# Performance work log

Hardware: AMD Instinct MI355X
Metric: run time of the kernel (lower is better)

## Reference

```python
import jax, jax.numpy as jnp
import numpy as np

N_EMBD = 1024
N_HEADS = 16
HEAD_DIM = N_EMBD // N_HEADS


def setup_inputs() -> dict:
    key = jax.random.key(0)
    k0, k1, k2, k3, k4 = jax.random.split(key, 5)
    scale = 1.0 / np.sqrt(N_EMBD)
    x = jax.random.normal(k0, (2, 2048, N_EMBD), dtype=jnp.float32)
    # nn.Linear(n_embd, 3*n_embd): weight [3d, d], bias [3d]
    w_qkv = jax.random.normal(k1, (3 * N_EMBD, N_EMBD), dtype=jnp.float32) * scale
    b_qkv = jax.random.normal(k2, (3 * N_EMBD,), dtype=jnp.float32) * scale
    w_proj = jax.random.normal(k3, (N_EMBD, N_EMBD), dtype=jnp.float32) * scale
    b_proj = jax.random.normal(k4, (N_EMBD,), dtype=jnp.float32) * scale
    return {"x": x, "w_qkv": w_qkv, "b_qkv": b_qkv, "w_proj": w_proj, "b_proj": b_proj}


def reference(x, w_qkv, b_qkv, w_proj, b_proj):
    b, l, d = x.shape
    h, f = N_HEADS, HEAD_DIM
    qkv = x @ w_qkv.T + b_qkv                      # [b, l, 3d]
    # rearrange 'b l (c h f) -> c b h l f'
    qkv = qkv.reshape(b, l, 3, h, f)
    q = jnp.transpose(qkv[:, :, 0], (0, 2, 1, 3))  # [b, h, l, f]
    k = jnp.transpose(qkv[:, :, 1], (0, 2, 1, 3))
    v = jnp.transpose(qkv[:, :, 2], (0, 2, 1, 3))
    scores = jnp.einsum('bhqf,bhkf->bhqk', q, k) / jnp.sqrt(jnp.float32(f))
    att = jax.nn.softmax(scores, axis=-1)          # [b, h, l, l]
    y = jnp.einsum('bhqk,bhkf->bhqf', att, v)      # [b, h, l, f]
    y = jnp.transpose(y, (0, 2, 1, 3)).reshape(b, l, d)  # 'b h l f -> b l (h f)'
    return y @ w_proj.T + b_proj
```

## Files before the change

### kernel.cpp

```cpp
#include <hip/hip_runtime.h>
#include <hip/hip_bf16.h>
#include <stdint.h>


typedef unsigned short u16;
typedef __attribute__((ext_vector_type(8))) short short8;
typedef __attribute__((ext_vector_type(4))) float f32x4;
typedef __attribute__((ext_vector_type(16))) float f32x16;
typedef __attribute__((ext_vector_type(4))) unsigned int u32x4;

#define MFMA16(a, b, c) __builtin_amdgcn_mfma_f32_16x16x32_bf16((a), (b), (c), 0, 0, 0)
#define MFMA32(a, b, c) __builtin_amdgcn_mfma_f32_32x32x16_bf16((a), (b), (c), 0, 0, 0)

__device__ __forceinline__ u16 f2bf(float x) {
  union { float f; uint32_t u; } v; v.f = x;
  uint32_t r = v.u + 0x7FFFu + ((v.u >> 16) & 1u);
  return (u16)(r >> 16);
}

__device__ __forceinline__ float fexp2(float x) {
#if __has_builtin(__builtin_amdgcn_exp2f)
  return __builtin_amdgcn_exp2f(x);
#else
  return exp2f(x);
#endif
}

__device__ __forceinline__ uint32_t pkbf(float lo, float hi) {
  uint32_t a = __builtin_bit_cast(uint32_t, lo) + 0x8000u;
  uint32_t b = __builtin_bit_cast(uint32_t, hi) + 0x8000u;
  return __builtin_amdgcn_perm(b, a, 0x07060302u);
}

__device__ __forceinline__ void gload16(const void* g, void* l) {
  __builtin_amdgcn_global_load_lds((const __attribute__((address_space(1))) void*)g,
                                   (__attribute__((address_space(3))) void*)l, 16, 0, 0);
}

__global__ __launch_bounds__(256) void cvt_all(const float* __restrict__ x,
                                               const float* __restrict__ wq,
                                               const float* __restrict__ wp,
                                               u16* __restrict__ xb,
                                               u16* __restrict__ wqb,
                                               u16* __restrict__ wpb) {
  int i = blockIdx.x * 256 + threadIdx.x;
  const float* s; u16* d; int off;
  if (i < 1048576) { s = x; d = xb; off = i; }
  else if (i < 1835008) { s = wq; d = wqb; off = i - 1048576; }
  else { s = wp; d = wpb; off = i - 1835008; }
  float4 f = reinterpret_cast<const float4*>(s)[off];
  ushort4 o;
  o.x = f2bf(f.x); o.y = f2bf(f.y); o.z = f2bf(f.z); o.w = f2bf(f.w);
  reinterpret_cast<ushort4*>(d)[off] = o;
}

template <int EPI>
__global__ __launch_bounds__(256, 4) void gemm_bt(const u16* __restrict__ A,
                                                  const u16* __restrict__ B,
                                                  const float* __restrict__ bias,
                                                  u16* __restrict__ outb,
                                                  float* __restrict__ outf,
                                                  int M, int N, int K) {
  __shared__ u16 smem[16384];
  const int tid = threadIdx.x;
  const int lane = tid & 63;
  const int wid = tid >> 6;
  const int bn = blockIdx.x, bm = blockIdx.y;
  const int row0 = bm * 128, col0 = bn * 128;
  const int wr = wid >> 1, wc = wid & 1;
  const int fr = lane & 15, fq = lane >> 4;

  f32x4 acc[4][4];
  #pragma unroll
  for (int m = 0; m < 4; m++)
    #pragma unroll
    for (int n = 0; n < 4; n++)
      #pragma unroll
      for (int j = 0; j < 4; j++) acc[m][n][j] = 0.f;

  const int cB = tid + 256;
  const int rA1 = tid >> 2, rA2 = cB >> 2;
  const int lA1 = (tid & 3) ^ ((tid >> 3) & 3);
  const int lA2 = (cB & 3) ^ ((cB >> 3) & 3);
  const size_t ga1 = (size_t)rA1 * K + lA1 * 8;
  const size_t ga2 = (size_t)rA2 * K + lA2 * 8;
  const int d1 = tid * 8, d2 = cB * 8;
  const u16* Ab = A + (size_t)row0 * K;
  const u16* Bb = B + (size_t)col0 * K;

  const int sl = (fq ^ ((fr >> 1) & 3)) * 8;
  const int niter = K >> 5;

  {
    u16* s = smem;
    gload16(Ab + ga1, s + d1);
    gload16(Ab + ga2, s + d2);
    gload16(Bb + ga1, s + 4096 + d1);
    gload16(Bb + ga2, s + 4096 + d2);
  }
  __syncthreads();

  for (int t = 0; t < niter; t++) {
    if (t + 1 < niter) {
      u16* s = smem + ((t + 1) & 1) * 8192;
      const size_t k0 = (size_t)(t + 1) * 32;
      gload16(Ab + ga1 + k0, s + d1);
      gload16(Ab + ga2 + k0, s + d2);
      gload16(Bb + ga1 + k0, s + 4096 + d1);
      gload16(Bb + ga2 + k0, s + 4096 + d2);
    }
    const u16* sa = smem + (t & 1) * 8192;
    const u16* sb = sa + 4096;
    short8 a[4], b[4];
    #pragma unroll
    for (int m = 0; m < 4; m++)
      a[m] = *(const short8*)&sa[(wr * 64 + m * 16 + fr) * 32 + sl];
    #pragma unroll
    for (int n = 0; n < 4; n++)
      b[n] = *(const short8*)&sb[(wc * 64 + n * 16 + fr) * 32 + sl];
    __builtin_amdgcn_s_setprio(1);
    #pragma unroll
    for (int m = 0; m < 4; m++)
      #pragma unroll
      for (int n = 0; n < 4; n++)
        acc[m][n] = MFMA16(a[m], b[n], acc[m][n]);
    __builtin_amdgcn_s_setprio(0);
    __syncthreads();
  }

  if (EPI == 0) {
    if (bn < 16) {
      #pragma unroll
      for (int m = 0; m < 4; m++) {
        #pragma unroll
        for (int n = 0; n < 4; n++) {
          #pragma unroll
          for (int j = 0; j < 4; j++) {
            int r = row0 + wr * 64 + m * 16 + fq * 4 + j;
            int c = col0 + wc * 64 + n * 16 + fr;
            float v = acc[m][n][j] + bias[c];
            int d = c & 1023, h = d >> 6, f = d & 63;
            int bb = r >> 11, ll = r & 2047;
            int bhh = bb * 16 + h;
            if (bn < 8) {
              outb[((size_t)bhh * 2048 + ll) * 64 + f] = f2bf(v * 0.18033688f);
            } else {
              outb[4194304u + ((size_t)bhh * 2048 + ll) * 64 + f] = f2bf(v);
            }
          }
        }
      }
    } else {
      u16* sC = smem;
      #pragma unroll
      for (int m = 0; m < 4; m++) {
        #pragma unroll
        for (int n = 0; n < 4; n++) {
          int c_local = wc * 64 + n * 16 + fr;
          int r_base = wr * 64 + m * 16 + fq * 4;
          float bi = bias[col0 + c_local];
          uint2 w;
          w.x = pkbf(acc[m][n][0] + bi, acc[m][n][1] + bi);
          w.y = pkbf(acc[m][n][2] + bi, acc[m][n][3] + bi);
          *(uint2*)&sC[c_local * 128 + (r_base ^ ((c_local & 7) << 3))] = w;
        }
      }
      __syncthreads();
      const int h0 = (col0 - 2048) >> 6;
      const int ll0 = row0 & 2047;
      const int bb = row0 >> 11;
      #pragma unroll
      for (int it = 0; it < 8; it++) {
        int chunk = tid + it * 256;
        int row_c = chunk >> 4, off = chunk & 15;
        short8 v = *(const short8*)&sC[row_c * 128 + ((off * 8) ^ ((row_c & 7) << 3))];
        int h = h0 + (row_c >> 6), f = row_c & 63;
        *(short8*)&outb[8388608u + ((size_t)((bb * 16 + h) * 64 + f)) * 2048 + ll0 + off * 8] = v;
      }
    }
  } else {
    #pragma unroll
    for (int m = 0; m < 4; m++)
      #pragma unroll
      for (int n = 0; n < 4; n++)
        #pragma unroll
        for (int j = 0; j < 4; j++) {
          int r = row0 + wr * 64 + m * 16 + fq * 4 + j;
          int c = col0 + wc * 64 + n * 16 + fr;
          outf[(size_t)r * N + c] = acc[m][n][j] + bias[c];
        }
  }
}

__device__ __forceinline__ void softpack1(const f32x16& st, float& lp,
                                          short8& paA, short8& paB) {
  float e[16];
  #pragma unroll
  for (int r = 0; r < 16; r++) e[r] = fexp2(st[r]);
  #pragma unroll
  for (int r = 0; r < 16; r++) lp += e[r];
  #pragma unroll
  for (int cc = 0; cc < 2; cc++) {
    uint32_t g0 = pkbf(e[8 * cc + 0], e[8 * cc + 1]);
    uint32_t g1 = pkbf(e[8 * cc + 2], e[8 * cc + 3]);
    uint32_t g2 = pkbf(e[8 * cc + 4], e[8 * cc + 5]);
    uint32_t g3 = pkbf(e[8 * cc + 6], e[8 * cc + 7]);
    asm volatile("v_permlane32_swap_b32 %0, %1" : "+v"(g0), "+v"(g2));
    asm volatile("v_permlane32_swap_b32 %0, %1" : "+v"(g1), "+v"(g3));
    u32x4 t;
    t[0] = g0; t[1] = g1; t[2] = g2; t[3] = g3;
    if (cc == 0) paA = __builtin_bit_cast(short8, t);
    else paB = __builtin_bit_cast(short8, t);
  }
}

__global__ __launch_bounds__(256, 4) void attn_kernel(const u16* __restrict__ qg,
                                                      const u16* __restrict__ kg,
                                                      const u16* __restrict__ vtg,
                                                      u16* __restrict__ y) {
  __shared__ u16 sStage[16384];
  __shared__ float sL2[64];
  const int x = blockIdx.x;
  const int bh = (x & 7) * 4 + (x >> 8);
  const int qt = (x >> 3) & 31;
  const int tid = threadIdx.x, l = tid & 63, wid = tid >> 6;
  const int qs = wid & 1, kh = wid >> 1;
  const int col = l & 31, hi = l >> 5;
  const size_t base = (size_t)bh * 131072;
  const u16* qp = qg + base;
  const u16* kp = kg + base + (size_t)kh * 1024 * 64;
  const u16* vp = vtg + base + (size_t)kh * 1024;
  const int qrow = qt * 64 + qs * 32;

  short8 qf[4];
  #pragma unroll
  for (int kk = 0; kk < 4; kk++)
    qf[kk] = *(const short8*)&qp[(size_t)(qrow + col) * 64 + kk * 16 + hi * 8];

  const int kc_row = tid >> 3;
  const int kc_src = kc_row * 64 + (((tid & 7) ^ ((tid >> 3) & 7)) * 8);
  const int vc_row = tid >> 2;
  const int vc_src = vc_row * 2048 + (((tid & 3) ^ ((tid >> 3) & 3)) * 8);
  const int kdst = tid * 8;
  const int vdst = 2048 + tid * 8;
  u16* S0 = sStage;
  u16* S1 = sStage + 8192;
  const u16* kp0 = kg + base;
  const u16* kp1 = kg + base + 65536;
  const u16* vp0 = vtg + base;
  const u16* vp1 = vtg + base + 1024;

  f32x16 o0, o1;
  float lp = 0.f;
  #pragma unroll
  for (int r = 0; r < 16; r++) { o0[r] = 0.f; o1[r] = 0.f; }

  const int krsw = (col & 7) << 3;
  const int vrsw = ((col >> 1) & 3) << 3;

  gload16(kp0 + kc_src, S0 + kdst);
  gload16(vp0 + vc_src, S0 + vdst);
  gload16(kp1 + kc_src, S1 + kdst);
  gload16(vp1 + vc_src, S1 + vdst);

  const u16* Sw = sStage + kh * 8192;
  int sel = 0;
  for (int t = 0; t < 32; t++) {
    __syncthreads();
    if (t + 1 < 32) {
      const size_t ko = (size_t)(t + 1) * 32 * 64;
      const int vo = (t + 1) * 32;
      u16* b0 = S0 + (sel ^ 1) * 4096;
      u16* b1 = S1 + (sel ^ 1) * 4096;
      gload16(kp0 + ko + kc_src, b0 + kdst);
      gload16(vp0 + vo + vc_src, b0 + vdst);
      gload16(kp1 + ko + kc_src, b1 + kdst);
      gload16(vp1 + vo + vc_src, b1 + vdst);
    }
    const u16* S = Sw + sel * 4096;

    f32x16 st;
    #pragma unroll
    for (int r = 0; r < 16; r++) st[r] = 0.f;
    __builtin_amdgcn_s_setprio(1);
    #pragma unroll
    for (int kk = 0; kk < 4; kk++) {
      short8 kb = *(const short8*)&S[col * 64 + ((kk * 16 + hi * 8) ^ krsw)];
      st = MFMA32(kb, qf[kk], st);
    }
    __builtin_amdgcn_s_setprio(0);

    short8 pa[2];
    softpack1(st, lp, pa[0], pa[1]);

    __builtin_amdgcn_s_setprio(1);
    #pragma unroll
    for (int c = 0; c < 2; c++) {
      short8 vb0 = *(const short8*)&S[2048 + col * 32 + ((c * 16 + hi * 8) ^ vrsw)];
      short8 vb1 = *(const short8*)&S[2048 + (32 + col) * 32 + ((c * 16 + hi * 8) ^ vrsw)];
      o0 = MFMA32(pa[c], vb0, o0);
      o1 = MFMA32(pa[c], vb1, o1);
    }
    __builtin_amdgcn_s_setprio(0);
    sel ^= 1;
  }

  __syncthreads();
  float* sM = (float*)sStage;
  float* sMl = sM + 4096;
  if (kh == 1) {
    #pragma unroll
    for (int r = 0; r < 16; r++) {
      sM[qs * 2048 + r * 64 + l] = o0[r];
      sM[qs * 2048 + (16 + r) * 64 + l] = o1[r];
    }
    sMl[qs * 64 + l] = lp;
  }
  __syncthreads();
  if (kh == 0) {
    #pragma unroll
    for (int r = 0; r < 16; r++) {
      o0[r] += sM[qs * 2048 + r * 64 + l];
      o1[r] += sM[qs * 2048 + (16 + r) * 64 + l];
    }
    lp += sMl[qs * 64 + l];
    float lsum = lp + __shfl_xor(lp, 32);
    if (l < 32) sL2[qs * 32 + col] = 1.0f / lsum;
    __builtin_amdgcn_s_waitcnt(0);
    const int b = bh >> 4, hh = bh & 15;
    #pragma unroll
    for (int fvt = 0; fvt < 2; fvt++) {
      #pragma unroll
      for (int r = 0; r < 16; r++) {
        int q = (r & 3) + 8 * (r >> 2) + 4 * hi;
        float li = sL2[qs * 32 + q];
        float v = (fvt == 0 ? o0[r] : o1[r]) * li;
        y[((size_t)(b * 2048 + qrow + q)) * 1024 + hh * 64 + fvt * 32 + col] = f2bf(v);
      }
    }
  }
}

extern "C" void kernel_launch(void* const* d_in, const int* in_sizes, int n_in,
                              void* d_out, int out_size, void* d_ws, size_t ws_size,
                              hipStream_t stream) {
  const float* x = (const float*)d_in[0];
  const float* w_qkv = (const float*)d_in[1];
  const float* b_qkv = (const float*)d_in[2];
  const float* w_proj = (const float*)d_in[3];
  const float* b_proj = (const float*)d_in[4];
  float* out = (float*)d_out;

  u16* ws = (u16*)d_ws;
  u16* xb = ws;
  u16* wq = xb + 4194304;
  u16* wp = wq + 3145728;
  u16* qb = wp + 1048576;
  u16* kb = qb + 4194304;
  u16* vb = kb + 4194304;
  u16* yb = vb + 4194304;

  cvt_all<<<8192, 256, 0, stream>>>(x, w_qkv, w_proj, xb, wq, wp);

  gemm_bt<0><<<dim3(24, 32), 256, 0, stream>>>(xb, wq, b_qkv, qb, nullptr, 4096, 3072, 1024);

  attn_kernel<<<1024, 256, 0, stream>>>(qb, kb, vb, yb);

  gemm_bt<1><<<dim3(8, 32), 256, 0, stream>>>(yb, wp, b_proj, nullptr, out, 4096, 1024, 1024);
}
```

Before: 121.8 us.

## Use four-slot K/V ring buffer and software-pipeline QK with softmax

Replaces the double-buffered K/V staging with a four-slot ring in shared memory. The loop now processes two tiles per iteration with one barrier, issuing the score MFMA for the next tile before the current softmax/PV so matrix work overlaps exp and packing. The row-sum accumulation is also rewritten as a balanced tree to shorten the dependency chain. Shared memory per block doubles, which can lower how many blocks fit per CU under the launch bound of four.

New measurement: 125.4 us. 3.0% more time.

```diff
diff --git a/kernel.cpp b/kernel.cpp
--- a/kernel.cpp
+++ b/kernel.cpp
@@ -197,8 +197,11 @@
   float e[16];
   #pragma unroll
   for (int r = 0; r < 16; r++) e[r] = fexp2(st[r]);
-  #pragma unroll
-  for (int r = 0; r < 16; r++) lp += e[r];
+  float s0 = (e[0] + e[1]) + (e[2] + e[3]);
+  float s1 = (e[4] + e[5]) + (e[6] + e[7]);
+  float s2 = (e[8] + e[9]) + (e[10] + e[11]);
+  float s3 = (e[12] + e[13]) + (e[14] + e[15]);
+  lp += (s0 + s1) + (s2 + s3);
   #pragma unroll
   for (int cc = 0; cc < 2; cc++) {
     uint32_t g0 = pkbf(e[8 * cc + 0], e[8 * cc + 1]);
@@ -218,7 +221,7 @@
                                                       const u16* __restrict__ kg,
                                                       const u16* __restrict__ vtg,
                                                       u16* __restrict__ y) {
-  __shared__ u16 sStage[16384];
+  __shared__ u16 sStage[32768];
   __shared__ float sL2[64];
   const int x = blockIdx.x;
   const int bh = (x & 7) * 4 + (x >> 8);
@@ -228,8 +231,6 @@
   const int col = l & 31, hi = l >> 5;
   const size_t base = (size_t)bh * 131072;
   const u16* qp = qg + base;
-  const u16* kp = kg + base + (size_t)kh * 1024 * 64;
-  const u16* vp = vtg + base + (size_t)kh * 1024;
   const int qrow = qt * 64 + qs * 32;
 
   short8 qf[4];
@@ -237,14 +238,12 @@
   for (int kk = 0; kk < 4; kk++)
     qf[kk] = *(const short8*)&qp[(size_t)(qrow + col) * 64 + kk * 16 + hi * 8];
 
-  const int kc_row = tid >> 3;
-  const int kc_src = kc_row * 64 + (((tid & 7) ^ ((tid >> 3) & 7)) * 8);
-  const int vc_row = tid >> 2;
-  const int vc_src = vc_row * 2048 + (((tid & 3) ^ ((tid >> 3) & 3)) * 8);
+  const int kc_src = (tid >> 3) * 64 + (((tid & 7) ^ ((tid >> 3) & 7)) * 8);
+  const int vc_src = (tid >> 2) * 2048 + (((tid & 3) ^ ((tid >> 3) & 3)) * 8);
   const int kdst = tid * 8;
   const int vdst = 2048 + tid * 8;
-  u16* S0 = sStage;
-  u16* S1 = sStage + 8192;
+  u16* R0 = sStage;
+  u16* R1 = sStage + 16384;
   const u16* kp0 = kg + base;
   const u16* kp1 = kg + base + 65536;
   const u16* vp0 = vtg + base;
@@ -257,28 +256,21 @@
 
   const int krsw = (col & 7) << 3;
   const int vrsw = ((col >> 1) & 3) << 3;
-
-  gload16(kp0 + kc_src, S0 + kdst);
-  gload16(vp0 + vc_src, S0 + vdst);
-  gload16(kp1 + kc_src, S1 + kdst);
-  gload16(vp1 + vc_src, S1 + vdst);
-
-  const u16* Sw = sStage + kh * 8192;
-  int sel = 0;
-  for (int t = 0; t < 32; t++) {
-    __syncthreads();
-    if (t + 1 < 32) {
-      const size_t ko = (size_t)(t + 1) * 32 * 64;
-      const int vo = (t + 1) * 32;
-      u16* b0 = S0 + (sel ^ 1) * 4096;
-      u16* b1 = S1 + (sel ^ 1) * 4096;
-      gload16(kp0 + ko + kc_src, b0 + kdst);
-      gload16(vp0 + vo + vc_src, b0 + vdst);
-      gload16(kp1 + ko + kc_src, b1 + kdst);
-      gload16(vp1 + vo + vc_src, b1 + vdst);
-    }
-    const u16* S = Sw + sel * 4096;
-
+  const u16* Rw = sStage + kh * 16384;
+
+  auto STAGE = [&](int tt) {
+    u16* b0 = R0 + (tt & 3) * 4096;
+    u16* b1 = R1 + (tt & 3) * 4096;
+    const size_t ko = (size_t)tt * 2048;
+    const int vo = tt * 32;
+    gload16(kp0 + ko + kc_src, b0 + kdst);
+    gload16(vp0 + vo + vc_src, b0 + vdst);
+    gload16(kp1 + ko + kc_src, b1 + kdst);
+    gload16(vp1 + vo + vc_src, b1 + vdst);
+  };
+
+  auto QK = [&](int tt) -> f32x16 {
+    const u16* S = Rw + (tt & 3) * 4096;
     f32x16 st;
     #pragma unroll
     for (int r = 0; r < 16; r++) st[r] = 0.f;
@@ -289,23 +281,39 @@
       st = MFMA32(kb, qf[kk], st);
     }
     __builtin_amdgcn_s_setprio(0);
-
-    short8 pa[2];
-    softpack1(st, lp, pa[0], pa[1]);
-
+    return st;
+  };
+
+  auto PV = [&](int tt, short8* pa) {
+    const u16* S = Rw + (tt & 3) * 4096 + 2048;
     __builtin_amdgcn_s_setprio(1);
     #pragma unroll
     for (int c = 0; c < 2; c++) {
-      short8 vb0 = *(const short8*)&S[2048 + col * 32 + ((c * 16 + hi * 8) ^ vrsw)];
-      short8 vb1 = *(const short8*)&S[2048 + (32 + col) * 32 + ((c * 16 + hi * 8) ^ vrsw)];
+      short8 vb0 = *(const short8*)&S[col * 32 + ((c * 16 + hi * 8) ^ vrsw)];
+      short8 vb1 = *(const short8*)&S[(32 + col) * 32 + ((c * 16 + hi * 8) ^ vrsw)];
       o0 = MFMA32(pa[c], vb0, o0);
       o1 = MFMA32(pa[c], vb1, o1);
     }
     __builtin_amdgcn_s_setprio(0);
-    sel ^= 1;
-  }
-
+  };
+
+  STAGE(0); STAGE(1); STAGE(2); STAGE(3);
   __syncthreads();
+  f32x16 stA = QK(0), stB;
+  short8 pa[2];
+
+  for (int t = 0; t < 32; t += 2) {
+    stB = QK(t + 1);
+    softpack1(stA, lp, pa[0], pa[1]);
+    PV(t, pa);
+    softpack1(stB, lp, pa[0], pa[1]);
+    PV(t + 1, pa);
+    __syncthreads();
+    if (t + 4 < 32) STAGE(t + 4);
+    if (t + 5 < 32) STAGE(t + 5);
+    if (t + 2 < 32) stA = QK(t + 2);
+  }
+
   float* sM = (float*)sStage;
   float* sMl = sM + 4096;
   if (kh == 1) {
```
